# Kernel optimization log

Measured on AMD Instinct MI355X. Metric: run time of the kernel, lower is better.

The kernel has to match this reference:

```python
import jax, jax.numpy as jnp
import numpy as np

B, S, D = 2, 2048, 1024
H = 16
HD = D // H  # 64


def setup_inputs() -> dict:
    key = jax.random.key(0)
    ks = jax.random.split(key, 9)
    s = 1.0 / np.sqrt(D)
    return {
        "query_input": jax.random.normal(ks[0], (B, S, D), dtype=jnp.float32),
        "Wq": jax.random.normal(ks[1], (D, D), dtype=jnp.float32) * s,
        "bq": jax.random.normal(ks[2], (D,), dtype=jnp.float32) * 0.02,
        "Wk": jax.random.normal(ks[3], (D, D), dtype=jnp.float32) * s,
        "bk": jax.random.normal(ks[4], (D,), dtype=jnp.float32) * 0.02,
        "Wv": jax.random.normal(ks[5], (D, D), dtype=jnp.float32) * s,
        "bv": jax.random.normal(ks[6], (D,), dtype=jnp.float32) * 0.02,
        "Wo": jax.random.normal(ks[7], (D, D), dtype=jnp.float32) * s,
        "bo": jax.random.normal(ks[8], (D,), dtype=jnp.float32) * 0.02,
    }


def _split_heads(x):
    # [B, S, D] -> [B, H, S, HD]
    return x.reshape(B, S, H, HD).transpose(0, 2, 1, 3)


def reference(query_input, Wq, bq, Wk, bk, Wv, bv, Wo, bo):
    # self-attention: key_value_input = query_input
    q = _split_heads(query_input @ Wq + bq)
    k = _split_heads(query_input @ Wk + bk)
    v = _split_heads(query_input @ Wv + bv)
    scores = jnp.einsum("bhqd,bhkd->bhqk", q, k) / jnp.sqrt(jnp.float32(HD))
    probs = jax.nn.softmax(scores, axis=-1)  # dropout is identity in eval
    ctx = jnp.einsum("bhqk,bhkd->bhqd", probs, v)
    ctx = ctx.transpose(0, 2, 1, 3).reshape(B, S, D)
    return ctx @ Wo + bo
```

## Files before the change

### kernel.cpp

```cpp
#include <hip/hip_runtime.h>
#include <hip/hip_bf16.h>
#include <cstdint>

constexpr int Bsz = 2, Seq = 2048, Dim = 1024, NH = 16, HDim = 64;
constexpr int Mtok = Bsz * Seq;
constexpr int NQKV = 3 * Dim;
constexpr float QSCALE = 0.125f * 1.4426950408889634f;

typedef __attribute__((ext_vector_type(4))) float f32x4;
typedef __attribute__((ext_vector_type(16))) float f32x16;
typedef __attribute__((ext_vector_type(8))) short bf16x8;

#if __has_builtin(__builtin_amdgcn_exp2f)
#define EXP2(x) __builtin_amdgcn_exp2f(x)
#else
#define EXP2(x) exp2f(x)
#endif

__device__ __forceinline__ ushort f2bf(float f) {
    union { float f; uint32_t u; } v; v.f = f;
    uint32_t u = v.u;
    uint32_t r = (u + 0x7fffu + ((u >> 16) & 1u)) >> 16;
    return (ushort)r;
}

__device__ __forceinline__ uint cvt_pk_bf16(float lo, float hi) {
    uint r;
    asm("v_cvt_pk_bf16_f32 %0, %1, %2" : "=v"(r) : "v"(lo), "v"(hi));
    return r;
}

__device__ __forceinline__ void gll16(const ushort* g, ushort* l) {
    __builtin_amdgcn_global_load_lds(
        (const __attribute__((address_space(1))) void*)g,
        (__attribute__((address_space(3))) void*)l, 16, 0, 0);
}

__global__ __launch_bounds__(256) void prep(const float* __restrict__ X,
                                            const float* __restrict__ Wq, const float* __restrict__ Wk,
                                            const float* __restrict__ Wv, const float* __restrict__ Wo,
                                            const float* __restrict__ bq, const float* __restrict__ bk,
                                            const float* __restrict__ bv,
                                            ushort* __restrict__ Xb, ushort* __restrict__ Wtqkv,
                                            ushort* __restrict__ Wto, float* __restrict__ bqkv) {
    __shared__ float tile[32][33];
    const int bid = blockIdx.x, tid = threadIdx.x;
    if (bid < 1024) {
        int i = bid * 256 + tid;
        const float4* p = (const float4*)X + (size_t)i * 4;
        float4 a = p[0], b = p[1], c2 = p[2], d = p[3];
        uint4 o0, o1;
        o0.x = (uint)f2bf(a.x) | ((uint)f2bf(a.y) << 16);
        o0.y = (uint)f2bf(a.z) | ((uint)f2bf(a.w) << 16);
        o0.z = (uint)f2bf(b.x) | ((uint)f2bf(b.y) << 16);
        o0.w = (uint)f2bf(b.z) | ((uint)f2bf(b.w) << 16);
        o1.x = (uint)f2bf(c2.x) | ((uint)f2bf(c2.y) << 16);
        o1.y = (uint)f2bf(c2.z) | ((uint)f2bf(c2.w) << 16);
        o1.z = (uint)f2bf(d.x) | ((uint)f2bf(d.y) << 16);
        o1.w = (uint)f2bf(d.z) | ((uint)f2bf(d.w) << 16);
        uint4* dst = (uint4*)Xb + (size_t)i * 2;
        dst[0] = o0;
        dst[1] = o1;
    } else if (bid < 5120) {
        int zb = bid - 1024;
        int z = zb >> 10, r2 = zb & 1023;
        int bx = (r2 & 31) * 32, by = (r2 >> 5) * 32;
        const float* src = (z == 0) ? Wq : (z == 1) ? Wk : (z == 2) ? Wv : Wo;
        ushort* dst = (z == 3) ? Wto : Wtqkv + (size_t)z * 1024 * 1024;
        float scale = (z == 0) ? QSCALE : 1.f;
        int tx = tid & 31, ty = tid >> 5;
#pragma unroll
        for (int j = 0; j < 32; j += 8)
            tile[ty + j][tx] = src[(size_t)(by + ty + j) * Dim + bx + tx];
        __syncthreads();
#pragma unroll
        for (int j = 0; j < 32; j += 8) {
            int n = bx + ty + j;
            dst[(size_t)n * Dim + by + tx] = f2bf(tile[tx][ty + j] * scale);
        }
    } else {
        int i = (bid - 5120) * 256 + tid;
        float v = (i < 1024) ? bq[i] * QSCALE : (i < 2048 ? bk[i - 1024] : bv[i - 2048]);
        bqkv[i] = v;
    }
}

__global__ __launch_bounds__(512, 2) void gemm_qkv(const ushort* __restrict__ A,
                                                   const ushort* __restrict__ Bt,
                                                   const float* __restrict__ bias,
                                                   ushort* __restrict__ Qp,
                                                   ushort* __restrict__ Kp,
                                                   ushort* __restrict__ Vp) {
    __shared__ ushort Al[2][2][8192];
    __shared__ ushort Bl[2][2][8192];
    const int tid = threadIdx.x;
    const int lane = tid & 63, wid = tid >> 6;
    const int wm = wid >> 2, wn = wid & 3;
    const int g = lane >> 4, r16 = lane & 15;
    const int sw = r16 & 7;
    const int lin = blockIdx.x + blockIdx.y * 16;
    const int swz = (lin & 7) * 24 + (lin >> 3);
    const int by = swz >> 4;
    const int bm = (swz & 15) * 256, bn = by * 256;
    const int srow = tid >> 3;
    const int gch = (tid & 7) ^ (srow & 7);
    const int wofs = wid * 512;

    const ushort* gAb = A  + (size_t)(bm + srow) * 1024 + gch * 8;
    const ushort* gBb = Bt + (size_t)(bn + srow) * 1024 + gch * 8;

#define STAGE_A(buf, h, t) do {                                          \
        const ushort* s_ = gAb + (size_t)(h) * 131072 + (t) * 64;        \
        gll16(s_,         &Al[buf][h][wofs]);                            \
        gll16(s_ + 65536, &Al[buf][h][4096 + wofs]);                     \
    } while (0)
#define STAGE_B(buf, h, t) do {                                          \
        const ushort* s_ = gBb + (size_t)(h) * 131072 + (t) * 64;        \
        gll16(s_,         &Bl[buf][h][wofs]);                            \
        gll16(s_ + 65536, &Bl[buf][h][4096 + wofs]);                     \
    } while (0)
#define LDA(buf, mi, ks) (*(const bf16x8*)&Al[buf][wm][((mi)*16 + r16) * 64 + ((((ks)*4 + g) ^ sw) * 8)])
#define LDB(buf, ni, ks) (*(const bf16x8*)&Bl[buf][wn >> 1][((wn & 1) * 64 + (ni)*16 + r16) * 64 + ((((ks)*4 + g) ^ sw) * 8)])

    f32x4 acc[8][4] = {};
    bf16x8 a0[4][2], a1[4][2], bA[2][2], bB[2][2];

    STAGE_A(0, 0, 0); STAGE_A(0, 1, 0); STAGE_B(0, 0, 0); STAGE_B(0, 1, 0);
    STAGE_A(1, 0, 1); STAGE_A(1, 1, 1); STAGE_B(1, 0, 1); STAGE_B(1, 1, 1);
    asm volatile("s_waitcnt vmcnt(8)" ::: "memory");
    __builtin_amdgcn_s_barrier();
    __builtin_amdgcn_sched_barrier(0);

#pragma unroll 2
    for (int t = 0; t < 16; ++t) {
        const int buf = t & 1;
#pragma unroll
        for (int mi = 0; mi < 4; mi++) { a0[mi][0] = LDA(buf, mi, 0); a0[mi][1] = LDA(buf, mi, 1); }
#pragma unroll
        for (int ni = 0; ni < 2; ni++) { bA[ni][0] = LDB(buf, ni, 0); bA[ni][1] = LDB(buf, ni, 1); }
        __builtin_amdgcn_s_setprio(1);
#pragma unroll
        for (int mi = 0; mi < 4; mi++)
#pragma unroll
            for (int ni = 0; ni < 2; ni++)
#pragma unroll
                for (int ks = 0; ks < 2; ks++)
                    acc[mi][ni] = __builtin_amdgcn_mfma_f32_16x16x32_bf16(a0[mi][ks], bA[ni][ks], acc[mi][ni], 0, 0, 0);
        __builtin_amdgcn_s_setprio(0);
#pragma unroll
        for (int ni = 0; ni < 2; ni++) { bB[ni][0] = LDB(buf, 2 + ni, 0); bB[ni][1] = LDB(buf, 2 + ni, 1); }
        __builtin_amdgcn_s_setprio(1);
#pragma unroll
        for (int mi = 0; mi < 4; mi++)
#pragma unroll
            for (int ni = 0; ni < 2; ni++)
#pragma unroll
                for (int ks = 0; ks < 2; ks++)
                    acc[mi][2 + ni] = __builtin_amdgcn_mfma_f32_16x16x32_bf16(a0[mi][ks], bB[ni][ks], acc[mi][2 + ni], 0, 0, 0);
        __builtin_amdgcn_s_setprio(0);
        __builtin_amdgcn_s_barrier();
        __builtin_amdgcn_sched_barrier(0);
#pragma unroll
        for (int mi = 0; mi < 4; mi++) { a1[mi][0] = LDA(buf, 4 + mi, 0); a1[mi][1] = LDA(buf, 4 + mi, 1); }
        if (t + 2 < 16) { STAGE_B(buf, 0, t + 2); STAGE_B(buf, 1, t + 2); }
        __builtin_amdgcn_s_setprio(1);
#pragma unroll
        for (int mi = 0; mi < 4; mi++)
#pragma unroll
            for (int ni = 0; ni < 2; ni++)
#pragma unroll
                for (int ks = 0; ks < 2; ks++)
                    acc[4 + mi][2 + ni] = __builtin_amdgcn_mfma_f32_16x16x32_bf16(a1[mi][ks], bB[ni][ks], acc[4 + mi][2 + ni], 0, 0, 0);
        __builtin_amdgcn_s_setprio(0);
        __builtin_amdgcn_s_barrier();
        __builtin_amdgcn_sched_barrier(0);
        if (t + 2 < 16) { STAGE_A(buf, 0, t + 2); STAGE_A(buf, 1, t + 2); }
        __builtin_amdgcn_s_setprio(1);
#pragma unroll
        for (int mi = 0; mi < 4; mi++)
#pragma unroll
            for (int ni = 0; ni < 2; ni++)
#pragma unroll
                for (int ks = 0; ks < 2; ks++)
                    acc[4 + mi][ni] = __builtin_amdgcn_mfma_f32_16x16x32_bf16(a1[mi][ks], bA[ni][ks], acc[4 + mi][ni], 0, 0, 0);
        __builtin_amdgcn_s_setprio(0);
        if (t + 2 < 16) asm volatile("s_waitcnt vmcnt(8)" ::: "memory");
        else            asm volatile("s_waitcnt vmcnt(0)" ::: "memory");
        __builtin_amdgcn_s_barrier();
        __builtin_amdgcn_sched_barrier(0);
    }
#undef STAGE_A
#undef STAGE_B
#undef LDA
#undef LDB

#pragma unroll
    for (int ni = 0; ni < 4; ni++) {
        const int col = bn + wn * 64 + ni * 16 + r16;
        const float bv = bias[col];
        if (by < 4) {
#pragma unroll
            for (int mi = 0; mi < 8; mi++) {
                int row0 = bm + wm * 128 + mi * 16 + g * 4;
                f32x4 c = acc[mi][ni];
#pragma unroll
                for (int i = 0; i < 4; i++)
                    Qp[(size_t)(row0 + i) * 1024 + col] = f2bf(c[i] + bv);
            }
        } else if (by < 8) {
            int h = ((bn - 1024) >> 6) + wn;
            int d = ni * 16 + r16;
#pragma unroll
            for (int mi = 0; mi < 8; mi++) {
                int row0 = bm + wm * 128 + mi * 16 + g * 4;
                f32x4 c = acc[mi][ni];
#pragma unroll
                for (int i = 0; i < 4; i++) {
                    int row = row0 + i;
                    int b = row >> 11, s = row & 2047;
                    size_t idx = ((size_t)(b * 16 + h) * 2048 + s) * 64
                               + (((d >> 3) ^ (s & 7)) << 3) + (d & 7);
                    Kp[idx] = f2bf(c[i] + bv);
                }
            }
        } else {
            int h = ((bn - 2048) >> 6) + wn;
            int dv = ni * 16 + r16;
#pragma unroll
            for (int mi = 0; mi < 8; mi++) {
                int row0 = bm + wm * 128 + mi * 16 + g * 4;
                f32x4 c = acc[mi][ni];
                int b = row0 >> 11, s = row0 & 2047;
                int s0 = s & ~63, si = s & 63;
                uint2 pk;
                pk.x = cvt_pk_bf16(c[0] + bv, c[1] + bv);
                pk.y = cvt_pk_bf16(c[2] + bv, c[3] + bv);
                size_t idx = ((size_t)(b * 16 + h) * 2048 + s0) * 64 + dv * 64
                           + (((si >> 3) ^ (dv & 7)) << 3) + (si & 7);
                *(uint2*)(Vp + idx) = pk;
            }
        }
    }
}

__global__ __launch_bounds__(256) void gemm_bt(const ushort* __restrict__ A,
                                               const ushort* __restrict__ Bt,
                                               const float* __restrict__ bias,
                                               float* __restrict__ Cout,
                                               int Nsz, int Ksz) {
    __shared__ ushort As[2][128 * 32];
    __shared__ ushort Bs[2][128 * 32];
    const int tid = threadIdx.x;
    const int lane = tid & 63, wid = tid >> 6;
    const int wm = wid >> 1, wn = wid & 1;
    const int lin = blockIdx.x + blockIdx.y * 32;
    const int swz = (lin & 7) * 32 + (lin >> 3);
    const int bm = (swz & 31) * 128, bn = (swz >> 5) * 128;
    const int g = lane >> 4, r16 = lane & 15;

    f32x4 acc[4][4] = {};

    const int srow = tid >> 2;
    const int sc = (tid & 3) ^ (srow & 3);
    const ushort* ga0 = A + (size_t)(bm + srow) * Ksz + sc * 8;
    const ushort* ga1 = A + (size_t)(bm + 64 + srow) * Ksz + sc * 8;
    const ushort* gb0 = Bt + (size_t)(bn + srow) * Ksz + sc * 8;
    const ushort* gb1 = Bt + (size_t)(bn + 64 + srow) * Ksz + sc * 8;
    const int lofs = wid << 9;

#define GSTAGE(bufi, k_)  do {                          \
        gll16(ga0 + (k_), &As[bufi][lofs]);             \
        gll16(ga1 + (k_), &As[bufi][2048 + lofs]);      \
        gll16(gb0 + (k_), &Bs[bufi][lofs]);             \
        gll16(gb1 + (k_), &Bs[bufi][2048 + lofs]);      \
    } while (0)

    GSTAGE(0, 0);
    int cur = 0;

    for (int k0 = 0; k0 < Ksz; k0 += 32) {
        __syncthreads();
        if (k0 + 32 < Ksz) GSTAGE(cur ^ 1, k0 + 32);
        const ushort* Asb = As[cur];
        const ushort* Bsb = Bs[cur];
        bf16x8 af[4], bfr[4];
#pragma unroll
        for (int mt = 0; mt < 4; mt++) {
            int row = wm * 64 + mt * 16 + r16;
            af[mt] = *(const bf16x8*)(Asb + row * 32 + ((g ^ (row & 3)) * 8));
        }
#pragma unroll
        for (int nt = 0; nt < 4; nt++) {
            int row = wn * 64 + nt * 16 + r16;
            bfr[nt] = *(const bf16x8*)(Bsb + row * 32 + ((g ^ (row & 3)) * 8));
        }
#pragma unroll
        for (int mt = 0; mt < 4; mt++)
#pragma unroll
            for (int nt = 0; nt < 4; nt++)
                acc[mt][nt] = __builtin_amdgcn_mfma_f32_16x16x32_bf16(af[mt], bfr[nt], acc[mt][nt], 0, 0, 0);
        cur ^= 1;
    }
#undef GSTAGE

#pragma unroll
    for (int nt = 0; nt < 4; nt++) {
        int col = bn + wn * 64 + nt * 16 + r16;
        float bv = bias[col];
#pragma unroll
        for (int mt = 0; mt < 4; mt++) {
            int row0 = bm + wm * 64 + mt * 16 + g * 4;
            f32x4 c = acc[mt][nt];
#pragma unroll
            for (int i = 0; i < 4; i++)
                Cout[(size_t)(row0 + i) * Nsz + col] = c[i] + bv;
        }
    }
}

__global__ __launch_bounds__(256) void attn(const ushort* __restrict__ Qp,
                                            const ushort* __restrict__ Kp,
                                            const ushort* __restrict__ Vp,
                                            ushort* __restrict__ Ctx) {
    __shared__ ushort Ks[3][4096];
    __shared__ ushort Vs[3][4096];
    __shared__ float Rl[4][32];
    const int tid = threadIdx.x, lane = tid & 63, w = tid >> 6;
    const int lin = blockIdx.x + blockIdx.y * 16;
    const int swz = (lin & 7) * 64 + (lin >> 3);
    const int bxl = swz & 15, bh = swz >> 4;
    const int b = bh >> 4, h = bh & 15;
    const int l31 = lane & 31, hi = lane >> 5, sw7 = l31 & 7;
    const bool lo = (hi == 0);
    const int qrow = bxl * 128 + w * 32;

    const ushort* Qr = Qp + (size_t)(b * Seq + qrow + l31) * 1024 + h * 64;
    bf16x8 qf[4];
#pragma unroll
    for (int ks = 0; ks < 4; ks++)
        qf[ks] = *(const bf16x8*)(Qr + ks * 16 + hi * 8);

    const ushort* KpB = Kp + (size_t)bh * Seq * 64;
    const ushort* VpB = Vp + (size_t)bh * Seq * 64;
    const int wb = w * 512;

    f32x16 M8;
#pragma unroll
    for (int r = 0; r < 16; r++) M8[r] = -8.f;

#define STAGE(slot, kv0_)  do {                                        \
        const ushort* ks_ = KpB + (size_t)(kv0_) * 64 + tid * 8;       \
        const ushort* vs_ = VpB + (size_t)(kv0_) * 64 + tid * 8;       \
        gll16(ks_,        &Ks[slot][wb]);                              \
        gll16(ks_ + 2048, &Ks[slot][2048 + wb]);                       \
        gll16(vs_,        &Vs[slot][wb]);                              \
        gll16(vs_ + 2048, &Vs[slot][2048 + wb]);                       \
    } while (0)

    f32x16 c0 = {}, c1 = {};
    float l_run = 0.f;

    auto QKT = [&](const ushort* Kt, f32x16& d0, f32x16& d1) {
        __builtin_amdgcn_s_setprio(1);
        {
            int ch = ((hi) ^ sw7) << 3;
            bf16x8 k0 = *(const bf16x8*)(Kt + l31 * 64 + ch);
            bf16x8 k1 = *(const bf16x8*)(Kt + (32 + l31) * 64 + ch);
            d0 = __builtin_amdgcn_mfma_f32_32x32x16_bf16(k0, qf[0], M8, 0, 0, 0);
            d1 = __builtin_amdgcn_mfma_f32_32x32x16_bf16(k1, qf[0], M8, 0, 0, 0);
        }
#pragma unroll
        for (int ks = 1; ks < 4; ks++) {
            int ch = ((ks * 2 + hi) ^ sw7) << 3;
            bf16x8 k0 = *(const bf16x8*)(Kt + l31 * 64 + ch);
            bf16x8 k1 = *(const bf16x8*)(Kt + (32 + l31) * 64 + ch);
            d0 = __builtin_amdgcn_mfma_f32_32x32x16_bf16(k0, qf[ks], d0, 0, 0, 0);
            d1 = __builtin_amdgcn_mfma_f32_32x32x16_bf16(k1, qf[ks], d1, 0, 0, 0);
        }
        __builtin_amdgcn_s_setprio(0);
    };
    auto SOFTPV = [&](const f32x16& s0, const f32x16& s1, const ushort* Vt) {
        float p0[16], p1[16];
        float ls = 0.f;
#pragma unroll
        for (int r = 0; r < 16; r++) {
            p0[r] = EXP2(s0[r]);
            p1[r] = EXP2(s1[r]);
            ls += p0[r] + p1[r];
        }
        l_run += ls;
        bf16x8 pa[4];
#pragma unroll
        for (int sl = 0; sl < 4; sl++) {
            const float* pp = (sl < 2) ? p0 : p1;
            int rb = (sl & 1) * 8;
            uint x  = cvt_pk_bf16(pp[rb + 0], pp[rb + 1]);
            uint x2 = cvt_pk_bf16(pp[rb + 2], pp[rb + 3]);
            uint y  = cvt_pk_bf16(pp[rb + 4], pp[rb + 5]);
            uint y2 = cvt_pk_bf16(pp[rb + 6], pp[rb + 7]);
            asm("v_permlane32_swap_b32 %0, %1" : "+v"(x),  "+v"(y));
            asm("v_permlane32_swap_b32 %0, %1" : "+v"(x2), "+v"(y2));
            union { uint u[4]; bf16x8 v; } fr;
            fr.u[0] = x;
            fr.u[1] = x2;
            fr.u[2] = y;
            fr.u[3] = y2;
            pa[sl] = fr.v;
        }
        __builtin_amdgcn_s_setprio(1);
#pragma unroll
        for (int sl = 0; sl < 4; sl++) {
            int ch = ((sl * 2 + hi) ^ sw7) << 3;
            bf16x8 vf0 = *(const bf16x8*)(Vt + l31 * 64 + ch);
            bf16x8 vf1 = *(const bf16x8*)(Vt + (32 + l31) * 64 + ch);
            c0 = __builtin_amdgcn_mfma_f32_32x32x16_bf16(pa[sl], vf0, c0, 0, 0, 0);
            c1 = __builtin_amdgcn_mfma_f32_32x32x16_bf16(pa[sl], vf1, c1, 0, 0, 0);
        }
        __builtin_amdgcn_s_setprio(0);
    };

    STAGE(0, 0);
    STAGE(1, 64);
    __syncthreads();
    f32x16 sA0, sA1, sB0, sB1;
    QKT(Ks[0], sA0, sA1);

    int sa = 0, sb = 1, scs = 2;
    for (int t = 0; t < 32; t += 2) {
        __syncthreads();
        if (t + 2 < 32) STAGE(scs, (t + 2) * 64);
        QKT(Ks[sb], sB0, sB1);
        SOFTPV(sA0, sA1, Vs[sa]);
        __syncthreads();
        if (t + 3 < 32) STAGE(sa, (t + 3) * 64);
        if (t + 2 < 32) QKT(Ks[scs], sA0, sA1);
        SOFTPV(sB0, sB1, Vs[sb]);
        int tmp = sa; sa = scs; scs = sb; sb = tmp;
    }
#undef STAGE

    float lt = l_run + __shfl_xor(l_run, 32);
    if (lo) Rl[w][l31] = 1.f / lt;
    __builtin_amdgcn_s_waitcnt(0);
    float rlv[16];
#pragma unroll
    for (int r = 0; r < 16; r++)
        rlv[r] = Rl[w][(r & 3) + 8 * (r >> 2) + 4 * hi];

    const int rowbase = b * Seq + qrow;
#pragma unroll
    for (int r = 0; r < 16; r++) {
        int q = (r & 3) + 8 * (r >> 2) + 4 * hi;
        int row = rowbase + q;
        Ctx[(size_t)row * Dim + h * 64 + l31]      = f2bf(c0[r] * rlv[r]);
        Ctx[(size_t)row * Dim + h * 64 + 32 + l31] = f2bf(c1[r] * rlv[r]);
    }
}

extern "C" void kernel_launch(void* const* d_in, const int* in_sizes, int n_in,
                              void* d_out, int out_size, void* d_ws, size_t ws_size,
                              hipStream_t stream) {
    const float* X  = (const float*)d_in[0];
    const float* Wq = (const float*)d_in[1];
    const float* bq = (const float*)d_in[2];
    const float* Wk = (const float*)d_in[3];
    const float* bk = (const float*)d_in[4];
    const float* Wv = (const float*)d_in[5];
    const float* bv = (const float*)d_in[6];
    const float* Wo = (const float*)d_in[7];
    const float* bo = (const float*)d_in[8];

    char* ws = (char*)d_ws;
    ushort* Xb    = (ushort*)(ws);
    ushort* Wtqkv = (ushort*)(ws + 8388608);
    ushort* Wto   = (ushort*)(ws + 14680064);
    float*  bqkv  = (float*)(ws + 16777216);
    ushort* Qp    = (ushort*)(ws + 16793600);
    ushort* Kp    = (ushort*)(ws + 25182208);
    ushort* Vp    = (ushort*)(ws + 33570816);
    ushort* Ctxb  = (ushort*)(ws + 41959424);

    prep<<<5132, 256, 0, stream>>>(X, Wq, Wk, Wv, Wo, bq, bk, bv, Xb, Wtqkv, Wto, bqkv);
    gemm_qkv<<<dim3(16, 12), 512, 0, stream>>>(Xb, Wtqkv, bqkv, Qp, Kp, Vp);
    attn<<<dim3(16, 32), 256, 0, stream>>>(Qp, Kp, Vp, Ctxb);
    gemm_bt<<<dim3(32, 8), 256, 0, stream>>>(Ctxb, Wto, bo, (float*)d_out, Dim, Dim);
}
```

Before: 119.6 us.

## Split attention into single-wave blocks with per-wave double-buffered KV staging

The attention kernel moves from 256-thread blocks (4 waves sharing a K/V tile) to 64-thread single-wave blocks, each owning 32 query rows and loading its own K/V tiles. A two-slot double buffer with vmcnt waits replaces the three-slot software pipeline and the __syncthreads barriers, and the reciprocal row sums reuse the K buffer in LDS. The aim is to remove block-level synchronisation and raise occupancy, but each wave now fetches the full K/V stream, so K/V global and L2 traffic grows fourfold. The interleaving of QK^T with softmax/PV across tiles is also gone.

```diff
diff --git a/kernel.cpp b/kernel.cpp
--- a/kernel.cpp
+++ b/kernel.cpp
@@ -318,21 +318,20 @@
     }
 }
 
-__global__ __launch_bounds__(256) void attn(const ushort* __restrict__ Qp,
-                                            const ushort* __restrict__ Kp,
-                                            const ushort* __restrict__ Vp,
-                                            ushort* __restrict__ Ctx) {
-    __shared__ ushort Ks[3][4096];
-    __shared__ ushort Vs[3][4096];
-    __shared__ float Rl[4][32];
-    const int tid = threadIdx.x, lane = tid & 63, w = tid >> 6;
-    const int lin = blockIdx.x + blockIdx.y * 16;
-    const int swz = (lin & 7) * 64 + (lin >> 3);
-    const int bxl = swz & 15, bh = swz >> 4;
+__global__ __launch_bounds__(64) void attn(const ushort* __restrict__ Qp,
+                                           const ushort* __restrict__ Kp,
+                                           const ushort* __restrict__ Vp,
+                                           ushort* __restrict__ Ctx) {
+    __shared__ ushort Ks[2][4096];
+    __shared__ ushort Vs[2][4096];
+    const int lane = threadIdx.x;
+    const int lin = blockIdx.x + blockIdx.y * 64;
+    const int swz = (lin & 7) * 256 + (lin >> 3);
+    const int bxl = swz & 63, bh = swz >> 6;
     const int b = bh >> 4, h = bh & 15;
     const int l31 = lane & 31, hi = lane >> 5, sw7 = l31 & 7;
     const bool lo = (hi == 0);
-    const int qrow = bxl * 128 + w * 32;
+    const int qrow = bxl * 32;
 
     const ushort* Qr = Qp + (size_t)(b * Seq + qrow + l31) * 1024 + h * 64;
     bf16x8 qf[4];
@@ -342,19 +341,19 @@
 
     const ushort* KpB = Kp + (size_t)bh * Seq * 64;
     const ushort* VpB = Vp + (size_t)bh * Seq * 64;
-    const int wb = w * 512;
 
     f32x16 M8;
 #pragma unroll
     for (int r = 0; r < 16; r++) M8[r] = -8.f;
 
-#define STAGE(slot, kv0_)  do {                                        \
-        const ushort* ks_ = KpB + (size_t)(kv0_) * 64 + tid * 8;       \
-        const ushort* vs_ = VpB + (size_t)(kv0_) * 64 + tid * 8;       \
-        gll16(ks_,        &Ks[slot][wb]);                              \
-        gll16(ks_ + 2048, &Ks[slot][2048 + wb]);                       \
-        gll16(vs_,        &Vs[slot][wb]);                              \
-        gll16(vs_ + 2048, &Vs[slot][2048 + wb]);                       \
+#define STAGE(slot, tile_)  do {                                        \
+        const ushort* ks_ = KpB + (size_t)(tile_) * 4096 + lane * 8;    \
+        const ushort* vs_ = VpB + (size_t)(tile_) * 4096 + lane * 8;    \
+        _Pragma("unroll")                                               \
+        for (int j = 0; j < 8; j++) {                                   \
+            gll16(ks_ + j * 512, &Ks[slot][j * 512]);                   \
+            gll16(vs_ + j * 512, &Vs[slot][j * 512]);                   \
+        }                                                               \
     } while (0)
 
     f32x16 c0 = {}, c1 = {};
@@ -419,33 +418,27 @@
         __builtin_amdgcn_s_setprio(0);
     };
 
+    f32x16 sA0, sA1;
     STAGE(0, 0);
-    STAGE(1, 64);
-    __syncthreads();
-    f32x16 sA0, sA1, sB0, sB1;
-    QKT(Ks[0], sA0, sA1);
-
-    int sa = 0, sb = 1, scs = 2;
-    for (int t = 0; t < 32; t += 2) {
-        __syncthreads();
-        if (t + 2 < 32) STAGE(scs, (t + 2) * 64);
-        QKT(Ks[sb], sB0, sB1);
-        SOFTPV(sA0, sA1, Vs[sa]);
-        __syncthreads();
-        if (t + 3 < 32) STAGE(sa, (t + 3) * 64);
-        if (t + 2 < 32) QKT(Ks[scs], sA0, sA1);
-        SOFTPV(sB0, sB1, Vs[sb]);
-        int tmp = sa; sa = scs; scs = sb; sb = tmp;
+    for (int t = 0; t < 32; ++t) {
+        const int cur = t & 1;
+        __builtin_amdgcn_sched_barrier(0);
+        asm volatile("s_waitcnt vmcnt(0)" ::: "memory");
+        __builtin_amdgcn_sched_barrier(0);
+        if (t + 1 < 32) STAGE(cur ^ 1, t + 1);
+        QKT(Ks[cur], sA0, sA1);
+        SOFTPV(sA0, sA1, Vs[cur]);
     }
 #undef STAGE
 
     float lt = l_run + __shfl_xor(l_run, 32);
-    if (lo) Rl[w][l31] = 1.f / lt;
+    float* RlP = (float*)&Ks[0][0];
+    if (lo) RlP[l31] = 1.f / lt;
     __builtin_amdgcn_s_waitcnt(0);
     float rlv[16];
 #pragma unroll
     for (int r = 0; r < 16; r++)
-        rlv[r] = Rl[w][(r & 3) + 8 * (r >> 2) + 4 * hi];
+        rlv[r] = RlP[(r & 3) + 8 * (r >> 2) + 4 * hi];
 
     const int rowbase = b * Seq + qrow;
 #pragma unroll
@@ -482,6 +475,6 @@
 
     prep<<<5132, 256, 0, stream>>>(X, Wq, Wk, Wv, Wo, bq, bk, bv, Xb, Wtqkv, Wto, bqkv);
     gemm_qkv<<<dim3(16, 12), 512, 0, stream>>>(Xb, Wtqkv, bqkv, Qp, Kp, Vp);
-    attn<<<dim3(16, 32), 256, 0, stream>>>(Qp, Kp, Vp, Ctxb);
+    attn<<<dim3(64, 32), 64, 0, stream>>>(Qp, Kp, Vp, Ctxb);
     gemm_bt<<<dim3(32, 8), 256, 0, stream>>>(Ctxb, Wto, bo, (float*)d_out, Dim, Dim);
 }
```

Result: slower. 164.2 us (+37.2%).
